# Kernel optimization log

Hardware: AMD Instinct MI355X
Metric: run time of the kernel (lower is better)

Reference implementation:

```python
import jax, jax.numpy as jnp
import numpy as np

TEMPERATURE = 0.1
EPS = 1e-12  # F.normalize default eps


def _l2norm(x):
    n = jnp.sqrt(jnp.sum(x * x, axis=-1, keepdims=True))
    return x / jnp.maximum(n, EPS)


def setup_inputs() -> dict:
    key = jax.random.key(0)
    k1, k2, k3 = jax.random.split(key, 3)
    G, NA, NO, D = 256, 256, 512, 128
    student_nodes = jax.random.normal(k1, (G * NA, D), dtype=jnp.float32)
    teacher_nodes = jax.random.normal(k2, (G * NO, D), dtype=jnp.float32)
    # local indices into each original graph's node block (as in t_nodes_all[kept_indices])
    kept_node_indices = jax.random.randint(k3, (G * NA,), 0, NO, dtype=jnp.int64)
    return {
        "student_nodes": student_nodes,
        "teacher_nodes": teacher_nodes,
        "kept_node_indices": kept_node_indices,
        "num_graphs": G,
        "n_aug": NA,
        "n_orig": NO,
    }


def reference(student_nodes, teacher_nodes, kept_node_indices, num_graphs, n_aug, n_orig):
    D = student_nodes.shape[-1]
    # ragged batch regularized: ptr boundaries -> fixed-size reshape
    s = _l2norm(student_nodes.reshape(num_graphs, n_aug, D))      # [G, Na, D]
    t = _l2norm(teacher_nodes.reshape(num_graphs, n_orig, D))     # [G, No, D]
    kept = kept_node_indices.reshape(num_graphs, n_aug)           # [G, Na]
    t_aligned = jnp.take_along_axis(t, kept[:, :, None], axis=1)  # [G, Na, D]
    scores = jnp.einsum("gid,gjd->gij", s, t_aligned) / TEMPERATURE  # [G, Na, Na]
    logp = jax.nn.log_softmax(scores, axis=-1)
    idx = jnp.arange(n_aug)
    # CE with labels = arange: -logp[g, i, i], mean over i per graph, then mean over graphs
    per_graph_ce = -jnp.mean(logp[:, idx, idx], axis=-1)          # [G]
    return jnp.mean(per_graph_ce)
```

## Files before the change

kernel.cpp:

```cpp
#include <hip/hip_runtime.h>
#include <hip/hip_bf16.h>

using f32x4  = __attribute__((ext_vector_type(4))) float;
using bf16x8 = __attribute__((ext_vector_type(8))) short;

constexpr int   G_NUM = 256;
constexpr int   NAUG  = 256;
constexpr int   NORIG = 512;
constexpr int   DIM   = 128;
constexpr float INV_T = 10.0f;

__device__ __forceinline__ short f32_to_bf16_bits(float x) {
    unsigned u = __float_as_uint(x);
    u += 0x7fffu + ((u >> 16) & 1u);
    return (short)(u >> 16);
}

__global__ __launch_bounds__(512, 4) void nlcl_main(
    const float* __restrict__ student,
    const float* __restrict__ teacher,
    const int*   __restrict__ kept,
    float*       __restrict__ block_sums)
{
    __shared__ short t_lds[NAUG * DIM];

    const int bid = blockIdx.x;
    const int logical = (bid & 7) * 64 + (bid >> 3);
    const int g    = logical >> 1;
    const int half = logical & 1;

    const int tid  = threadIdx.x;
    const int lane = tid & 63;
    const int wave = tid >> 6;
    const int rbase = half * 128;

    const float* s_base = student + (size_t)g * NAUG * DIM;
    const float* t_base = teacher + (size_t)g * NORIG * DIM;
    const int*   k_base = kept + g * NAUG;

    const int ccol  = lane & 15;
    const int cquad = lane >> 4;

    const int hw = tid >> 5;
    const int hl = tid & 31;
    int idxv[16];
    #pragma unroll
    for (int it = 0; it < 16; ++it) idxv[it] = k_base[it * 16 + hw];

    bf16x8 afrag[4];
    {
        const int row = rbase + wave * 16 + ccol;
        const float* rp = s_base + row * DIM;
        float sf[4][8];
        #pragma unroll
        for (int kc = 0; kc < 4; ++kc) {
            const int d0 = kc * 32 + cquad * 8;
            const float4 a = *reinterpret_cast<const float4*>(rp + d0);
            const float4 b = *reinterpret_cast<const float4*>(rp + d0 + 4);
            sf[kc][0] = a.x; sf[kc][1] = a.y; sf[kc][2] = a.z; sf[kc][3] = a.w;
            sf[kc][4] = b.x; sf[kc][5] = b.y; sf[kc][6] = b.z; sf[kc][7] = b.w;
        }
        float ss = 0.f;
        #pragma unroll
        for (int kc = 0; kc < 4; ++kc)
            #pragma unroll
            for (int e = 0; e < 8; ++e) ss += sf[kc][e] * sf[kc][e];
        ss += __shfl_xor(ss, 16);
        ss += __shfl_xor(ss, 32);
        const float scale = rsqrtf(fmaxf(ss, 1e-24f));
        #pragma unroll
        for (int kc = 0; kc < 4; ++kc)
            #pragma unroll
            for (int e = 0; e < 8; ++e)
                afrag[kc][e] = f32_to_bf16_bits(sf[kc][e] * scale);
    }

    {
        char* tl = reinterpret_cast<char*>(t_lds);
        #pragma unroll
        for (int it = 0; it < 16; ++it) {
            const int j   = it * 16 + hw;
            const float* rp = t_base + (size_t)idxv[it] * DIM;
            const float4 v = *reinterpret_cast<const float4*>(rp + hl * 4);
            float ss = v.x * v.x + v.y * v.y + v.z * v.z + v.w * v.w;
            ss += __shfl_xor(ss, 1);
            ss += __shfl_xor(ss, 2);
            ss += __shfl_xor(ss, 4);
            ss += __shfl_xor(ss, 8);
            ss += __shfl_xor(ss, 16);
            const float scale = rsqrtf(fmaxf(ss, 1e-24f));
            short4 o;
            o.x = f32_to_bf16_bits(v.x * scale);
            o.y = f32_to_bf16_bits(v.y * scale);
            o.z = f32_to_bf16_bits(v.z * scale);
            o.w = f32_to_bf16_bits(v.w * scale);
            const int byte = j * 256 + ((hl * 8) ^ ((j & 7) << 4));
            *reinterpret_cast<short4*>(tl + byte) = o;
        }
    }
    __syncthreads();

    float sumexp[4] = {0.f, 0.f, 0.f, 0.f};
    float diagsum = 0.f;
    const char* tl = reinterpret_cast<const char*>(t_lds);

    for (int ct = 0; ct < 16; ++ct) {
        f32x4 acc = {0.f, 0.f, 0.f, 0.f};
        const int j = ct * 16 + ccol;
        #pragma unroll
        for (int kc = 0; kc < 4; ++kc) {
            const int byte = j * 256 + (((kc * 64) + (cquad * 16)) ^ ((j & 7) << 4));
            const bf16x8 b = *reinterpret_cast<const bf16x8*>(tl + byte);
            acc = __builtin_amdgcn_mfma_f32_16x16x32_bf16(afrag[kc], b, acc, 0, 0, 0);
        }
        #pragma unroll
        for (int reg = 0; reg < 4; ++reg) {
            const int row = rbase + wave * 16 + cquad * 4 + reg;
            const float l = acc[reg] * INV_T;
            sumexp[reg] += __expf(l);
            if (j == row) diagsum += l;
        }
    }

    float ce = 0.f;
    #pragma unroll
    for (int reg = 0; reg < 4; ++reg) {
        float s = sumexp[reg];
        s += __shfl_xor(s, 1);
        s += __shfl_xor(s, 2);
        s += __shfl_xor(s, 4);
        s += __shfl_xor(s, 8);
        if (ccol == 0) ce += __logf(s);
    }
    ce -= diagsum;
    ce += __shfl_xor(ce, 1);
    ce += __shfl_xor(ce, 2);
    ce += __shfl_xor(ce, 4);
    ce += __shfl_xor(ce, 8);
    ce += __shfl_xor(ce, 16);
    ce += __shfl_xor(ce, 32);

    __syncthreads();
    float* red = reinterpret_cast<float*>(t_lds);
    if (lane == 0) red[wave] = ce;
    __syncthreads();
    if (tid == 0) {
        float t = 0.f;
        #pragma unroll
        for (int w = 0; w < 8; ++w) t += red[w];
        block_sums[bid] = t;
    }
}

__global__ void nlcl_reduce(const float* __restrict__ block_sums,
                            float* __restrict__ out)
{
    __shared__ float r[8];
    const int tid = threadIdx.x;
    float v = block_sums[tid];
    v += __shfl_xor(v, 1);
    v += __shfl_xor(v, 2);
    v += __shfl_xor(v, 4);
    v += __shfl_xor(v, 8);
    v += __shfl_xor(v, 16);
    v += __shfl_xor(v, 32);
    if ((tid & 63) == 0) r[tid >> 6] = v;
    __syncthreads();
    if (tid == 0) {
        float t = 0.f;
        #pragma unroll
        for (int w = 0; w < 8; ++w) t += r[w];
        out[0] = t * (1.0f / ((float)G_NUM * (float)NAUG));
    }
}

extern "C" void kernel_launch(void* const* d_in, const int* in_sizes, int n_in,
                              void* d_out, int out_size, void* d_ws, size_t ws_size,
                              hipStream_t stream) {
    (void)in_sizes; (void)n_in; (void)out_size; (void)ws_size;
    const float* student = (const float*)d_in[0];
    const float* teacher = (const float*)d_in[1];
    const int*   kept    = (const int*)d_in[2];
    float* bs  = (float*)d_ws;
    float* out = (float*)d_out;

    nlcl_main<<<512, 512, 0, stream>>>(student, teacher, kept, bs);
    nlcl_reduce<<<1, 512, 0, stream>>>(bs, out);
}
```

Measured before the change: 24.45 us.

## Defer L2 norm scaling to logits and software-pipeline teacher gather loads

Measured after the change: 25.13 us. 1.03x slower.

```diff
diff --git a/kernel.cpp b/kernel.cpp
--- a/kernel.cpp
+++ b/kernel.cpp
@@ -23,6 +23,9 @@
     float*       __restrict__ block_sums)
 {
     __shared__ short t_lds[NAUG * DIM];
+    __shared__ float rt_lds[NAUG];
+    __shared__ float rs_lds[128];
+    __shared__ float red[8];
 
     const int bid = blockIdx.x;
     const int logical = (bid & 7) * 64 + (bid >> 3);
@@ -43,80 +46,105 @@
 
     const int hw = tid >> 5;
     const int hl = tid & 31;
+
     int idxv[16];
     #pragma unroll
     for (int it = 0; it < 16; ++it) idxv[it] = k_base[it * 16 + hw];
+
+    const int srow = rbase + wave * 16 + ccol;
+    const float* rp = s_base + srow * DIM;
+    float4 sv[8];
+    #pragma unroll
+    for (int kc = 0; kc < 4; ++kc) {
+        sv[kc * 2]     = *reinterpret_cast<const float4*>(rp + kc * 32 + cquad * 8);
+        sv[kc * 2 + 1] = *reinterpret_cast<const float4*>(rp + kc * 32 + cquad * 8 + 4);
+    }
+
+    float4 gv0[4], gv1[4];
+    #pragma unroll
+    for (int i = 0; i < 4; ++i)
+        gv0[i] = *reinterpret_cast<const float4*>(t_base + (size_t)idxv[i] * DIM + hl * 4);
+    #pragma unroll
+    for (int i = 0; i < 4; ++i)
+        gv1[i] = *reinterpret_cast<const float4*>(t_base + (size_t)idxv[4 + i] * DIM + hl * 4);
 
     bf16x8 afrag[4];
     {
-        const int row = rbase + wave * 16 + ccol;
-        const float* rp = s_base + row * DIM;
-        float sf[4][8];
+        float ss = 0.f;
         #pragma unroll
         for (int kc = 0; kc < 4; ++kc) {
-            const int d0 = kc * 32 + cquad * 8;
-            const float4 a = *reinterpret_cast<const float4*>(rp + d0);
-            const float4 b = *reinterpret_cast<const float4*>(rp + d0 + 4);
-            sf[kc][0] = a.x; sf[kc][1] = a.y; sf[kc][2] = a.z; sf[kc][3] = a.w;
-            sf[kc][4] = b.x; sf[kc][5] = b.y; sf[kc][6] = b.z; sf[kc][7] = b.w;
-        }
-        float ss = 0.f;
-        #pragma unroll
-        for (int kc = 0; kc < 4; ++kc)
-            #pragma unroll
-            for (int e = 0; e < 8; ++e) ss += sf[kc][e] * sf[kc][e];
+            const float4 a = sv[kc * 2], b = sv[kc * 2 + 1];
+            afrag[kc][0] = f32_to_bf16_bits(a.x); afrag[kc][1] = f32_to_bf16_bits(a.y);
+            afrag[kc][2] = f32_to_bf16_bits(a.z); afrag[kc][3] = f32_to_bf16_bits(a.w);
+            afrag[kc][4] = f32_to_bf16_bits(b.x); afrag[kc][5] = f32_to_bf16_bits(b.y);
+            afrag[kc][6] = f32_to_bf16_bits(b.z); afrag[kc][7] = f32_to_bf16_bits(b.w);
+            ss += a.x * a.x + a.y * a.y + a.z * a.z + a.w * a.w;
+            ss += b.x * b.x + b.y * b.y + b.z * b.z + b.w * b.w;
+        }
         ss += __shfl_xor(ss, 16);
         ss += __shfl_xor(ss, 32);
-        const float scale = rsqrtf(fmaxf(ss, 1e-24f));
-        #pragma unroll
-        for (int kc = 0; kc < 4; ++kc)
+        if (cquad == 0)
+            rs_lds[wave * 16 + ccol] = rsqrtf(fmaxf(ss, 1e-24f)) * INV_T;
+    }
+
+    char* tl = reinterpret_cast<char*>(t_lds);
+    #pragma unroll
+    for (int c = 0; c < 4; ++c) {
+        float4 cur[4];
+        #pragma unroll
+        for (int i = 0; i < 4; ++i) cur[i] = (c & 1) ? gv1[i] : gv0[i];
+        if (c < 2) {
             #pragma unroll
-            for (int e = 0; e < 8; ++e)
-                afrag[kc][e] = f32_to_bf16_bits(sf[kc][e] * scale);
-    }
-
-    {
-        char* tl = reinterpret_cast<char*>(t_lds);
-        #pragma unroll
-        for (int it = 0; it < 16; ++it) {
-            const int j   = it * 16 + hw;
-            const float* rp = t_base + (size_t)idxv[it] * DIM;
-            const float4 v = *reinterpret_cast<const float4*>(rp + hl * 4);
+            for (int i = 0; i < 4; ++i) {
+                float4 nxt = *reinterpret_cast<const float4*>(
+                    t_base + (size_t)idxv[(c + 2) * 4 + i] * DIM + hl * 4);
+                if (c & 1) gv1[i] = nxt; else gv0[i] = nxt;
+            }
+        }
+        #pragma unroll
+        for (int i = 0; i < 4; ++i) {
+            const int it = c * 4 + i;
+            const int j  = it * 16 + hw;
+            const float4 v = cur[i];
+            short4 o;
+            o.x = f32_to_bf16_bits(v.x); o.y = f32_to_bf16_bits(v.y);
+            o.z = f32_to_bf16_bits(v.z); o.w = f32_to_bf16_bits(v.w);
+            const int byte = j * 256 + ((hl * 8) ^ ((j & 7) << 4));
+            *reinterpret_cast<short4*>(tl + byte) = o;
             float ss = v.x * v.x + v.y * v.y + v.z * v.z + v.w * v.w;
             ss += __shfl_xor(ss, 1);
             ss += __shfl_xor(ss, 2);
             ss += __shfl_xor(ss, 4);
             ss += __shfl_xor(ss, 8);
             ss += __shfl_xor(ss, 16);
-            const float scale = rsqrtf(fmaxf(ss, 1e-24f));
-            short4 o;
-            o.x = f32_to_bf16_bits(v.x * scale);
-            o.y = f32_to_bf16_bits(v.y * scale);
-            o.z = f32_to_bf16_bits(v.z * scale);
-            o.w = f32_to_bf16_bits(v.w * scale);
-            const int byte = j * 256 + ((hl * 8) ^ ((j & 7) << 4));
-            *reinterpret_cast<short4*>(tl + byte) = o;
+            if (hl == 0)
+                rt_lds[j] = rsqrtf(fmaxf(ss, 1e-24f));
         }
     }
     __syncthreads();
 
     float sumexp[4] = {0.f, 0.f, 0.f, 0.f};
     float diagsum = 0.f;
-    const char* tl = reinterpret_cast<const char*>(t_lds);
+    const char* tlc = reinterpret_cast<const char*>(t_lds);
+    float rs[4];
+    #pragma unroll
+    for (int reg = 0; reg < 4; ++reg)
+        rs[reg] = rs_lds[wave * 16 + cquad * 4 + reg];
 
     for (int ct = 0; ct < 16; ++ct) {
         f32x4 acc = {0.f, 0.f, 0.f, 0.f};
         const int j = ct * 16 + ccol;
+        const float rt = rt_lds[j];
         #pragma unroll
         for (int kc = 0; kc < 4; ++kc) {
             const int byte = j * 256 + (((kc * 64) + (cquad * 16)) ^ ((j & 7) << 4));
-            const bf16x8 b = *reinterpret_cast<const bf16x8*>(tl + byte);
+            const bf16x8 b = *reinterpret_cast<const bf16x8*>(tlc + byte);
             acc = __builtin_amdgcn_mfma_f32_16x16x32_bf16(afrag[kc], b, acc, 0, 0, 0);
         }
         #pragma unroll
         for (int reg = 0; reg < 4; ++reg) {
             const int row = rbase + wave * 16 + cquad * 4 + reg;
-            const float l = acc[reg] * INV_T;
+            const float l = acc[reg] * rs[reg] * rt;
             sumexp[reg] += __expf(l);
             if (j == row) diagsum += l;
         }
@@ -140,8 +168,6 @@
     ce += __shfl_xor(ce, 16);
     ce += __shfl_xor(ce, 32);
 
-    __syncthreads();
-    float* red = reinterpret_cast<float*>(t_lds);
     if (lane == 0) red[wave] = ce;
     __syncthreads();
     if (tid == 0) {
```
